# Kernel tuning notes

Hardware: AMD Instinct MI355X
Metric: run time of the kernel (lower is better)

The kernel has to match this reference:

```python
import jax, jax.numpy as jnp
import numpy as np

B, S, H = 2, 2048, 2304
NH, HD, NKV = 8, 256, 4
WINDOW = 512
CAP = 50.0
THETA = 10000.0
NEG_INF = -2.3819763e38


def setup_inputs() -> dict:
    key = jax.random.key(0)
    ks = jax.random.split(key, 6)
    hidden_states = jax.random.normal(ks[0], (B, S, H), dtype=jnp.float32)
    # causal additive mask (0 where attend, -inf-ish where masked)
    i = jnp.arange(S)
    causal = i[None, :] <= i[:, None]
    attention_mask = jnp.broadcast_to(
        jnp.where(causal, 0.0, NEG_INF).astype(jnp.float32)[None, None], (B, 1, S, S)
    )
    position_ids = jnp.broadcast_to(jnp.arange(S, dtype=jnp.int32)[None], (B, S))
    scale = 0.02
    Wq = jax.random.normal(ks[1], (H, NH * HD), dtype=jnp.float32) * scale
    Wk = jax.random.normal(ks[2], (H, NKV * HD), dtype=jnp.float32) * scale
    Wv = jax.random.normal(ks[3], (H, NKV * HD), dtype=jnp.float32) * scale
    Wo = jax.random.normal(ks[4], (NH * HD, H), dtype=jnp.float32) * scale
    return {
        "hidden_states": hidden_states,
        "attention_mask": attention_mask,
        "position_ids": position_ids,
        "Wq": Wq,
        "Wk": Wk,
        "Wv": Wv,
        "Wo": Wo,
    }


def _rotate_half(x):
    h = x.shape[-1] // 2
    return jnp.concatenate([-x[..., h:], x[..., :h]], axis=-1)


def reference(hidden_states, attention_mask, position_ids, Wq, Wk, Wv, Wo):
    b, s, _ = hidden_states.shape
    q = (hidden_states @ Wq).reshape(b, s, NH, HD).transpose(0, 2, 1, 3)   # [B,NH,S,HD]
    k = (hidden_states @ Wk).reshape(b, s, NKV, HD).transpose(0, 2, 1, 3)  # [B,NKV,S,HD]
    v = (hidden_states @ Wv).reshape(b, s, NKV, HD).transpose(0, 2, 1, 3)
    # rotary embedding
    inv_freq = 1.0 / (THETA ** (jnp.arange(0, HD, 2, dtype=jnp.float32) / HD))
    freqs = position_ids.astype(jnp.float32)[..., None] * inv_freq  # [B,S,HD/2]
    emb = jnp.concatenate([freqs, freqs], axis=-1)                  # [B,S,HD]
    cos = jnp.cos(emb)[:, None]  # unsqueeze head dim
    sin = jnp.sin(emb)[:, None]
    q = q * cos + _rotate_half(q) * sin
    k = k * cos + _rotate_half(k) * sin
    # GQA: repeat kv heads
    rep = NH // NKV
    k = jnp.repeat(k, rep, axis=1)
    v = jnp.repeat(v, rep, axis=1)
    logits = jnp.einsum("bhqd,bhkd->bhqk", q, k) / jnp.sqrt(jnp.float32(HD))
    # sliding-window mask: keep |i-j| <= WINDOW-1, else NEG_INF
    idx = jnp.arange(s)
    sliding = jnp.abs(idx[:, None] - idx[None, :]) <= (WINDOW - 1)
    mask = jnp.where(sliding[None, None], attention_mask, NEG_INF)
    # tanh logit softcapping, then additive mask
    logits = jnp.tanh(logits / CAP) * CAP + mask
    probs = jax.nn.softmax(logits.astype(jnp.float32), axis=-1).astype(q.dtype)
    out = jnp.einsum("bhqk,bhkd->bhqd", probs, v)
    out = out.transpose(0, 2, 1, 3).reshape(b, s, NH * HD)
    return out @ Wo
```

## Files before the change

### kernel.cpp

```cpp
#include <hip/hip_runtime.h>
#include <cmath>

#define B_   2
#define S_   2048
#define H_   2304
#define NH_  8
#define HD_  256
#define NKV_ 4
#define WIN_ 512
#define QKVW 4096

typedef unsigned short ushort_t;
typedef __attribute__((ext_vector_type(8))) short bf16x8;
typedef __attribute__((ext_vector_type(4))) float floatx4;
typedef __attribute__((ext_vector_type(16))) float floatx16;

__device__ __forceinline__ unsigned short f2bf(float f) {
  unsigned u = __builtin_bit_cast(unsigned, f);
  u += 0x7fff + ((u >> 16) & 1);
  return (unsigned short)(u >> 16);
}
__device__ __forceinline__ float bf2f(ushort_t v) {
  unsigned u = (unsigned)v << 16;
  return __builtin_bit_cast(float, u);
}

__device__ __forceinline__ void gl2lds16(const void* g, void* l) {
  __builtin_amdgcn_global_load_lds(
      (const __attribute__((address_space(1))) unsigned int*)g,
      (__attribute__((address_space(3))) unsigned int*)l, 16, 0, 0);
}

__global__ void cast_bf16(const float* __restrict__ in, ushort_t* __restrict__ out) {
  const int i = blockIdx.x * 256 + threadIdx.x;
  float4 v = ((const float4*)in)[i];
  ushort4 o;
  o.x = f2bf(v.x); o.y = f2bf(v.y); o.z = f2bf(v.z); o.w = f2bf(v.w);
  ((ushort4*)out)[i] = o;
}

__global__ void transpose_cast(const float* __restrict__ W, ushort_t* __restrict__ Wt,
                               int K, int N) {
  __shared__ float t[32][33];
  const int lx = threadIdx.x & 31, ly = threadIdx.x >> 5;
  const int n0 = blockIdx.x * 32, k0 = blockIdx.y * 32;
#pragma unroll
  for (int i = 0; i < 4; ++i)
    t[ly + i * 8][lx] = W[(long long)(k0 + ly + i * 8) * N + n0 + lx];
  __syncthreads();
#pragma unroll
  for (int i = 0; i < 4; ++i)
    Wt[(long long)(n0 + ly + i * 8) * K + k0 + lx] = f2bf(t[lx][ly + i * 8]);
}

template <bool OUT_BF16>
__launch_bounds__(256)
__global__ void gemm_bt(const ushort_t* __restrict__ A,
                        const ushort_t* __restrict__ Bt,
                        void* __restrict__ Cv, int M, int N, int K) {
  __shared__ ushort_t As[128 * 32];
  __shared__ ushort_t Bs[128 * 32];
  const int tid = threadIdx.x, lane = tid & 63, wid = tid >> 6;
  const int bm = blockIdx.y * 128, bn = blockIdx.x * 128;
  const int wm = (wid >> 1) * 64, wn = (wid & 1) * 64;

  floatx16 acc[2][2] = {};

  const int r = lane >> 2, c = lane & 3;
  const int skey = (r >> 1) & 3;
  const int scol = (c ^ skey) * 8;
  const int srow = wid * 32 + r;
  const long long aBase = (long long)(bm + srow) * K + scol;
  const long long bBase = (long long)(bn + srow) * K + scol;
  ushort_t* AsW = &As[(wid * 32) * 32];
  ushort_t* BsW = &Bs[(wid * 32) * 32];

  const int l31 = lane & 31, lg = lane >> 5;
  const int swz = (l31 >> 1) & 3;

  for (int k0 = 0; k0 < K; k0 += 32) {
    __syncthreads();
    gl2lds16(A + aBase + k0,           AsW);
    gl2lds16(A + aBase + k0 + 16 * K,  AsW + 16 * 32);
    gl2lds16(Bt + bBase + k0,          BsW);
    gl2lds16(Bt + bBase + k0 + 16 * K, BsW + 16 * 32);
    __syncthreads();

    bf16x8 af[2][2], bfr[2][2];
#pragma unroll
    for (int mt = 0; mt < 2; ++mt)
#pragma unroll
      for (int h = 0; h < 2; ++h) {
        af[mt][h]  = *(const bf16x8*)&As[(wm + 32 * mt + l31) * 32 + ((2 * h + lg) ^ swz) * 8];
        bfr[mt][h] = *(const bf16x8*)&Bs[(wn + 32 * mt + l31) * 32 + ((2 * h + lg) ^ swz) * 8];
      }
#pragma unroll
    for (int h = 0; h < 2; ++h)
#pragma unroll
      for (int mt = 0; mt < 2; ++mt)
#pragma unroll
        for (int nt = 0; nt < 2; ++nt)
          acc[mt][nt] = __builtin_amdgcn_mfma_f32_32x32x16_bf16(af[mt][h], bfr[nt][h],
                                                                acc[mt][nt], 0, 0, 0);
  }

#pragma unroll
  for (int mt = 0; mt < 2; ++mt)
#pragma unroll
    for (int nt = 0; nt < 2; ++nt) {
      const int col = bn + wn + 32 * nt + l31;
#pragma unroll
      for (int g = 0; g < 4; ++g)
#pragma unroll
        for (int rr = 0; rr < 4; ++rr) {
          const int row = bm + wm + 32 * mt + rr + 8 * g + 4 * lg;
          const float v = acc[mt][nt][g * 4 + rr];
          if (OUT_BF16) ((ushort_t*)Cv)[(long long)row * N + col] = f2bf(v);
          else          ((float*)Cv)[(long long)row * N + col]    = v;
        }
    }
}

__global__ void rope_inplace(ushort_t* __restrict__ QKV16, const int* __restrict__ pos) {
  const int bs  = blockIdx.x;
  const int gid = blockIdx.y * 256 + threadIdx.x;
  const int head = gid >> 7;
  const int d    = gid & 127;
  const float pp   = (float)pos[bs];
  const float invf = __expf(-(float)d * (9.210340371976184f / 128.0f));
  const float ang  = pp * invf;
  const float cc = cosf(ang), sn = sinf(ang);
  ushort_t* base = QKV16 + (size_t)bs * QKVW + head * HD_;
  const float x1 = bf2f(base[d]);
  const float x2 = bf2f(base[d + 128]);
  float o1 = x1 * cc - x2 * sn;
  float o2 = x2 * cc + x1 * sn;
  if (head < NH_) { o1 *= 0.0625f; o2 *= 0.0625f; }
  base[d]       = f2bf(o1);
  base[d + 128] = f2bf(o2);
}

__global__ void v_prep(const ushort_t* __restrict__ QKV16, ushort_t* __restrict__ Vt16) {
  __shared__ ushort_t tile[32][33];
  const int k0 = blockIdx.x * 32, d0 = blockIdx.y * 32;
  const int b = blockIdx.z >> 2, hk = blockIdx.z & 3;
  const int lx = threadIdx.x & 31, ly = threadIdx.x >> 5;
#pragma unroll
  for (int i = 0; i < 4; ++i)
    tile[ly + 8 * i][lx] =
        QKV16[(size_t)(b * S_ + k0 + ly + 8 * i) * QKVW + 3072 + hk * HD_ + d0 + lx];
  __syncthreads();
#pragma unroll
  for (int i = 0; i < 4; ++i)
    Vt16[((size_t)(b * NKV_ + hk) * HD_ + d0 + ly + 8 * i) * S_ + k0 + lx] =
        tile[lx][ly + 8 * i];
}

__launch_bounds__(512)
__global__ void attn_mfma(const ushort_t* __restrict__ QKV16,
                          const ushort_t* __restrict__ Vt16,
                          ushort_t* __restrict__ AOb) {
  __shared__ ushort_t Ks[32 * 256];
  __shared__ ushort_t Vts[256 * 32];
  __shared__ ushort_t Ps[8][16 * 32];
  __shared__ float rsb[8][16];

  const int lane = threadIdx.x & 63, w = threadIdx.x >> 6;
  const int l15 = lane & 15, lq = lane >> 4;
  const int qb = blockIdx.x * 64;
  const int hp = blockIdx.y, b = blockIdx.z;
  const int h  = hp * 2 + (w >> 2);
  const int hw = w & 3;

  const ushort_t* Qh = QKV16 + (size_t)b * S_ * QKVW + h * HD_;
  const ushort_t* Kh = QKV16 + (size_t)b * S_ * QKVW + 2048 + hp * HD_;
  const ushort_t* Vh = Vt16 + ((size_t)(b * NKV_ + hp) * HD_) * S_;

  const int qw = qb + hw * 16;

  bf16x8 afq[8];
  {
    const ushort_t* qr = Qh + (size_t)(qw + l15) * QKVW + lq * 8;
#pragma unroll
    for (int kd = 0; kd < 8; ++kd) afq[kd] = *(const bf16x8*)(qr + kd * 32);
  }

  floatx4 acc[16] = {};
  float rs[4] = {0.f, 0.f, 0.f, 0.f};

  int kb0 = qb - (WIN_ - 1);
  if (kb0 < 0) kb0 = 0;
  kb0 &= ~31;

  const int ksp = lane & 31, ksr = lane >> 5;
  const int vsp = lane & 3,  vsr = lane >> 2;

  for (int kb = kb0; kb < qb + 64; kb += 32) {
    __syncthreads();
#pragma unroll
    for (int i = 0; i < 2; ++i) {
      const int kl = w * 4 + 2 * i + ksr;
      gl2lds16(Kh + (size_t)(kb + kl) * QKVW + (ksp ^ (kl & 31)) * 8,
               &Ks[(w * 4 + 2 * i) * 256]);
    }
#pragma unroll
    for (int i = 0; i < 2; ++i) {
      const int dl = w * 32 + 16 * i + vsr;
      gl2lds16(Vh + (size_t)dl * S_ + kb + (vsp ^ ((dl >> 1) & 3)) * 8,
               &Vts[(w * 32 + 16 * i) * 32]);
    }
    __syncthreads();

    if (kb <= qw + 15 && kb + 31 >= qw - (WIN_ - 1)) {
      ushort_t* Pw = Ps[w];
#pragma unroll
      for (int kt = 0; kt < 2; ++kt) {
        floatx4 sacc = {};
        const int keyl = kt * 16 + l15;
        const int krow = keyl * 256;
        const int ksw = keyl & 31;
#pragma unroll
        for (int kd = 0; kd < 8; ++kd) {
          bf16x8 bk = *(const bf16x8*)&Ks[krow + ((kd * 4 + lq) ^ ksw) * 8];
          sacc = __builtin_amdgcn_mfma_f32_16x16x32_bf16(afq[kd], bk, sacc, 0, 0, 0);
        }
        const int keyg = kb + keyl;
#pragma unroll
        for (int rr = 0; rr < 4; ++rr) {
          const int qg = qw + lq * 4 + rr;
          const float t = __expf(sacc[rr] * 0.04f);
          const float L = 50.f - __fdividef(100.f, t + 1.f);
          float p = __expf(L);
          p = (keyg <= qg && keyg >= qg - (WIN_ - 1)) ? p : 0.f;
          rs[rr] += p;
          const int ql = lq * 4 + rr;
          const int ch = kt * 2 + (l15 >> 3);
          Pw[ql * 32 + ((ch ^ ((ql >> 1) & 3)) * 8) + (l15 & 7)] = f2bf(p);
        }
      }
      asm volatile("s_waitcnt lgkmcnt(0)" ::: "memory");

      const bf16x8 bp = *(const bf16x8*)&Pw[l15 * 32 + ((lq ^ ((l15 >> 1) & 3)) * 8)];
      const int vsw = (l15 >> 1) & 3;
#pragma unroll
      for (int t = 0; t < 16; ++t) {
        bf16x8 av = *(const bf16x8*)&Vts[(t * 16 + l15) * 32 + ((lq ^ vsw) * 8)];
        acc[t] = __builtin_amdgcn_mfma_f32_16x16x32_bf16(av, bp, acc[t], 0, 0, 0);
      }
    }
  }

#pragma unroll
  for (int rr = 0; rr < 4; ++rr) {
    rs[rr] += __shfl_xor(rs[rr], 1, 64);
    rs[rr] += __shfl_xor(rs[rr], 2, 64);
    rs[rr] += __shfl_xor(rs[rr], 4, 64);
    rs[rr] += __shfl_xor(rs[rr], 8, 64);
  }
  if (l15 == 0) {
#pragma unroll
    for (int rr = 0; rr < 4; ++rr) rsb[w][lq * 4 + rr] = rs[rr];
  }
  asm volatile("s_waitcnt lgkmcnt(0)" ::: "memory");
  __builtin_amdgcn_wave_barrier();
  const float inv = 1.0f / rsb[w][l15];

  const size_t ob = ((size_t)(b * S_ + qw + l15) * NH_ + h) * HD_;
#pragma unroll
  for (int t = 0; t < 16; ++t) {
    ushort4 o;
    o.x = f2bf(acc[t][0] * inv);
    o.y = f2bf(acc[t][1] * inv);
    o.z = f2bf(acc[t][2] * inv);
    o.w = f2bf(acc[t][3] * inv);
    *(ushort4*)&AOb[ob + t * 16 + lq * 4] = o;
  }
}

extern "C" void kernel_launch(void* const* d_in, const int* in_sizes, int n_in,
                              void* d_out, int out_size, void* d_ws, size_t ws_size,
                              hipStream_t stream) {
  const float* X   = (const float*)d_in[0];
  const int*   pos = (const int*)d_in[2];
  const float* Wq  = (const float*)d_in[3];
  const float* Wk  = (const float*)d_in[4];
  const float* Wv  = (const float*)d_in[5];
  const float* Wo  = (const float*)d_in[6];
  float* out = (float*)d_out;

  const int M  = B_ * S_;
  const int NQ = NH_ * HD_;
  const int NK = NKV_ * HD_;

  char* w = (char*)d_ws;
  ushort_t* QKV16 = (ushort_t*)w;  w += (size_t)M * QKVW * 2;
  ushort_t* Xb    = (ushort_t*)w;  w += (size_t)M * H_ * 2;
  ushort_t* Wqkvt = (ushort_t*)w;  w += (size_t)QKVW * H_ * 2;
  ushort_t* Wot   = (ushort_t*)w;  w += (size_t)H_ * NQ * 2;
  ushort_t* Vt16  = (ushort_t*)w;  w += (size_t)B_ * NKV_ * S_ * HD_ * 2;
  ushort_t* AOb   = (ushort_t*)w;  w += (size_t)M * NQ * 2;

  dim3 blk(256);

  cast_bf16<<<(M * H_) / 1024, blk, 0, stream>>>(X, Xb);
  transpose_cast<<<dim3(NQ / 32, H_ / 32), blk, 0, stream>>>(Wq, Wqkvt, H_, NQ);
  transpose_cast<<<dim3(NK / 32, H_ / 32), blk, 0, stream>>>(Wk, Wqkvt + (size_t)2048 * H_, H_, NK);
  transpose_cast<<<dim3(NK / 32, H_ / 32), blk, 0, stream>>>(Wv, Wqkvt + (size_t)3072 * H_, H_, NK);
  transpose_cast<<<dim3(H_ / 32, NQ / 32), blk, 0, stream>>>(Wo, Wot, NQ, H_);

  gemm_bt<true><<<dim3(QKVW / 128, M / 128), blk, 0, stream>>>(Xb, Wqkvt, QKV16, M, QKVW, H_);

  rope_inplace<<<dim3(M, 6), blk, 0, stream>>>(QKV16, pos);
  v_prep<<<dim3(S_ / 32, HD_ / 32, B_ * NKV_), blk, 0, stream>>>(QKV16, Vt16);

  attn_mfma<<<dim3(S_ / 64, NKV_, B_), dim3(512), 0, stream>>>(QKV16, Vt16, AOb);

  gemm_bt<false><<<dim3(H_ / 128, M / 128), blk, 0, stream>>>(AOb, Wot, out, M, H_, NQ);
}
```

Measured before the change: 406.4 us.

## Rewrite GEMM with register-prefetched K=64 tiles and 16x16x32 MFMA

Rewrites the bf16 GEMM main loop. K tiles grow from 32 to 64, and async global-to-LDS loads are replaced by register prefetch of the next tile that overlaps the MFMA work. The 32x32x16 MFMAs become a 4x4 grid of 16x16x32 MFMAs with a new XOR swizzle. The goal is to hide global latency and halve the barriers per K, at the cost of more registers and LDS per block.

Measured after the change: 381.1 us. 1.07x faster.

```diff
diff --git a/kernel.cpp b/kernel.cpp
--- a/kernel.cpp
+++ b/kernel.cpp
@@ -13,7 +13,6 @@
 typedef unsigned short ushort_t;
 typedef __attribute__((ext_vector_type(8))) short bf16x8;
 typedef __attribute__((ext_vector_type(4))) float floatx4;
-typedef __attribute__((ext_vector_type(16))) float floatx16;
 
 __device__ __forceinline__ unsigned short f2bf(float f) {
   unsigned u = __builtin_bit_cast(unsigned, f);
@@ -58,66 +57,81 @@
 __global__ void gemm_bt(const ushort_t* __restrict__ A,
                         const ushort_t* __restrict__ Bt,
                         void* __restrict__ Cv, int M, int N, int K) {
-  __shared__ ushort_t As[128 * 32];
-  __shared__ ushort_t Bs[128 * 32];
+  __shared__ ushort_t As[128 * 64];
+  __shared__ ushort_t Bs[128 * 64];
   const int tid = threadIdx.x, lane = tid & 63, wid = tid >> 6;
   const int bm = blockIdx.y * 128, bn = blockIdx.x * 128;
   const int wm = (wid >> 1) * 64, wn = (wid & 1) * 64;
 
-  floatx16 acc[2][2] = {};
-
-  const int r = lane >> 2, c = lane & 3;
-  const int skey = (r >> 1) & 3;
-  const int scol = (c ^ skey) * 8;
-  const int srow = wid * 32 + r;
-  const long long aBase = (long long)(bm + srow) * K + scol;
-  const long long bBase = (long long)(bn + srow) * K + scol;
-  ushort_t* AsW = &As[(wid * 32) * 32];
-  ushort_t* BsW = &Bs[(wid * 32) * 32];
-
-  const int l31 = lane & 31, lg = lane >> 5;
-  const int swz = (l31 >> 1) & 3;
-
-  for (int k0 = 0; k0 < K; k0 += 32) {
+  floatx4 acc[4][4] = {};
+
+  const int r  = tid >> 1;
+  const int cp = (tid & 1) * 4;
+  const int wkey = r & 7;
+  const ushort_t* Ap = A  + (long long)(bm + r) * K + cp * 8;
+  const ushort_t* Bp = Bt + (long long)(bn + r) * K + cp * 8;
+  ushort_t* Aw = &As[r * 64];
+  ushort_t* Bw = &Bs[r * 64];
+
+  const int l15 = lane & 15, lq = lane >> 4;
+  const int rkey = l15 & 7;
+
+  bf16x8 ar[4], br[4];
+#pragma unroll
+  for (int i = 0; i < 4; ++i) {
+    ar[i] = *(const bf16x8*)(Ap + i * 8);
+    br[i] = *(const bf16x8*)(Bp + i * 8);
+  }
+
+  for (int k0 = 0; k0 < K; k0 += 64) {
     __syncthreads();
-    gl2lds16(A + aBase + k0,           AsW);
-    gl2lds16(A + aBase + k0 + 16 * K,  AsW + 16 * 32);
-    gl2lds16(Bt + bBase + k0,          BsW);
-    gl2lds16(Bt + bBase + k0 + 16 * K, BsW + 16 * 32);
+#pragma unroll
+    for (int i = 0; i < 4; ++i) {
+      *(bf16x8*)&Aw[((cp + i) ^ wkey) * 8] = ar[i];
+      *(bf16x8*)&Bw[((cp + i) ^ wkey) * 8] = br[i];
+    }
     __syncthreads();
 
-    bf16x8 af[2][2], bfr[2][2];
-#pragma unroll
-    for (int mt = 0; mt < 2; ++mt)
-#pragma unroll
-      for (int h = 0; h < 2; ++h) {
-        af[mt][h]  = *(const bf16x8*)&As[(wm + 32 * mt + l31) * 32 + ((2 * h + lg) ^ swz) * 8];
-        bfr[mt][h] = *(const bf16x8*)&Bs[(wn + 32 * mt + l31) * 32 + ((2 * h + lg) ^ swz) * 8];
-      }
-#pragma unroll
-    for (int h = 0; h < 2; ++h)
-#pragma unroll
-      for (int mt = 0; mt < 2; ++mt)
-#pragma unroll
-        for (int nt = 0; nt < 2; ++nt)
-          acc[mt][nt] = __builtin_amdgcn_mfma_f32_32x32x16_bf16(af[mt][h], bfr[nt][h],
-                                                                acc[mt][nt], 0, 0, 0);
-  }
-
-#pragma unroll
-  for (int mt = 0; mt < 2; ++mt)
-#pragma unroll
-    for (int nt = 0; nt < 2; ++nt) {
-      const int col = bn + wn + 32 * nt + l31;
-#pragma unroll
-      for (int g = 0; g < 4; ++g)
-#pragma unroll
-        for (int rr = 0; rr < 4; ++rr) {
-          const int row = bm + wm + 32 * mt + rr + 8 * g + 4 * lg;
-          const float v = acc[mt][nt][g * 4 + rr];
-          if (OUT_BF16) ((ushort_t*)Cv)[(long long)row * N + col] = f2bf(v);
-          else          ((float*)Cv)[(long long)row * N + col]    = v;
-        }
+    if (k0 + 64 < K) {
+      const int kn = k0 + 64;
+#pragma unroll
+      for (int i = 0; i < 4; ++i) {
+        ar[i] = *(const bf16x8*)(Ap + kn + i * 8);
+        br[i] = *(const bf16x8*)(Bp + kn + i * 8);
+      }
+    }
+
+#pragma unroll
+    for (int kk = 0; kk < 2; ++kk) {
+      bf16x8 af[4], bfr[4];
+#pragma unroll
+      for (int i = 0; i < 4; ++i) {
+        af[i]  = *(const bf16x8*)&As[(wm + i * 16 + l15) * 64 + ((kk * 4 + lq) ^ rkey) * 8];
+        bfr[i] = *(const bf16x8*)&Bs[(wn + i * 16 + l15) * 64 + ((kk * 4 + lq) ^ rkey) * 8];
+      }
+#pragma unroll
+      for (int i = 0; i < 4; ++i)
+#pragma unroll
+        for (int j = 0; j < 4; ++j)
+          acc[i][j] = __builtin_amdgcn_mfma_f32_16x16x32_bf16(af[i], bfr[j], acc[i][j], 0, 0, 0);
+    }
+  }
+
+  const int r0 = lq * 4, c0 = l15;
+#pragma unroll
+  for (int i = 0; i < 4; ++i)
+#pragma unroll
+    for (int j = 0; j < 4; ++j) {
+      const long long base = (long long)(bm + wm + i * 16 + r0) * N + bn + wn + j * 16 + c0;
+      if (OUT_BF16) {
+        ushort_t* Cp = (ushort_t*)Cv + base;
+#pragma unroll
+        for (int rr = 0; rr < 4; ++rr) Cp[(long long)rr * N] = f2bf(acc[i][j][rr]);
+      } else {
+        float* Cp = (float*)Cv + base;
+#pragma unroll
+        for (int rr = 0; rr < 4; ++rr) Cp[(long long)rr * N] = acc[i][j][rr];
+      }
     }
 }
 
```
